# Kernel optimization log

Measured on AMD Instinct MI355X. Metric: run time of the kernel, lower is better.

The kernel has to match this reference:

```python
import jax, jax.numpy as jnp
import numpy as np

INPUT_SCALE = 1.0
TABLE_SIZE = 32
D_EMBED = 64
N = 1_000_000


def setup_inputs() -> dict:
    key = jax.random.key(0)
    k1, k2 = jax.random.split(key)
    x = jax.random.normal(k1, (N, 3), dtype=jnp.float32)
    # learned table parameter: [E, D, H, W] (batch dim of 1 dropped)
    table = jax.random.normal(k2, (D_EMBED, TABLE_SIZE, TABLE_SIZE, TABLE_SIZE), dtype=jnp.float32) * 0.1
    return {"x": x, "table": table}


def _grid_sample_3d(table, grid):
    """F.grid_sample(table[None], grid[None,None,None]) with mode='bilinear',
    padding_mode='zeros', align_corners=False.
    table: [E, D, H, W]; grid: [n, 3] with (x->W, y->H, z->D) order.
    Returns [n, E]."""
    E, Dz, Hy, Wx = table.shape
    sizes_f = jnp.array([Wx, Hy, Dz], dtype=table.dtype)
    dims_i = jnp.array([Wx, Hy, Dz], dtype=jnp.int32)
    # align_corners=False: pix = ((coord + 1) * size - 1) / 2
    pix = ((grid + 1.0) * sizes_f - 1.0) * 0.5   # [n, 3]
    p0f = jnp.floor(pix)
    frac = pix - p0f                              # [n, 3]
    p0 = p0f.astype(jnp.int32)
    tab_flat = table.reshape(E, -1).T             # [D*H*W, E]
    out = jnp.zeros((grid.shape[0], E), dtype=table.dtype)
    for dz in (0, 1):
        for dy in (0, 1):
            for dx in (0, 1):
                off = jnp.array([dx, dy, dz], dtype=jnp.int32)
                idx = p0 + off                                        # [n, 3]
                inb = jnp.all((idx >= 0) & (idx < dims_i), axis=-1)   # zeros padding
                idxc = jnp.clip(idx, 0, dims_i - 1)
                lin = (idxc[:, 2] * Hy + idxc[:, 1]) * Wx + idxc[:, 0]
                vals = tab_flat[lin]                                  # [n, E]
                w = jnp.prod(jnp.where(off == 1, frac, 1.0 - frac), axis=-1)
                out = out + vals * (w * inb.astype(table.dtype))[:, None]
    return out


def reference(x, table):
    xc = jnp.clip(x * INPUT_SCALE, -1.0, 1.0)
    return _grid_sample_3d(table, xc)
```

## Files before the change

kernel.cpp:

```cpp
#include <hip/hip_runtime.h>


constexpr int TSZ = 32;
constexpr int S   = TSZ * TSZ * TSZ;
constexpr int EMB = 64;

typedef float floatx4 __attribute__((ext_vector_type(4)));
typedef float f32x2   __attribute__((ext_vector_type(2)));

__device__ __forceinline__ unsigned short f32_to_bf16_rne(float f) {
  unsigned int u = __float_as_uint(f);
  unsigned int lsb = (u >> 16) & 1u;
  u += 0x7FFFu + lsb;
  return (unsigned short)(u >> 16);
}

__global__ __launch_bounds__(256) void transpose_table_k(
    const float* __restrict__ tab, unsigned short* __restrict__ tabT) {
  __shared__ float tile[EMB][EMB + 1];
  const int s_base = blockIdx.x * 64;
  const int t  = threadIdx.x;
  const int c0 = t & 63;
  const int r0 = t >> 6;
#pragma unroll
  for (int i = 0; i < 16; ++i) {
    const int e = r0 + 4 * i;
    tile[e][c0] = tab[(size_t)e * S + (s_base + c0)];
  }
  __syncthreads();
  const int hv = c0 >> 5;
  const int ch = c0 & 31;
#pragma unroll
  for (int i = 0; i < 16; ++i) {
    const int s = r0 + 4 * i;
    tabT[(size_t)hv * S * 32 + (size_t)(s_base + s) * 32 + ch] =
        f32_to_bf16_rne(tile[c0][s]);
  }
}

__global__ __launch_bounds__(256) void embed_k(
    const float* __restrict__ x, const uint4* __restrict__ tabT,
    float* __restrict__ out, int n, int nchunks) {
  const int bid = blockIdx.x;
  const int hv    = (bid >> 2) & 1;
  const int chunk = (bid >> 3) * 4 + (bid & 3);
  if (chunk >= nchunks) return;
  const int t  = threadIdx.x;
  const int pt = chunk * 64 + (t >> 2);
  if (pt >= n) return;
  const int o  = t & 3;

  const float gx = fminf(fmaxf(__builtin_nontemporal_load(&x[3 * pt + 0]), -1.f), 1.f);
  const float gy = fminf(fmaxf(__builtin_nontemporal_load(&x[3 * pt + 1]), -1.f), 1.f);
  const float gz = fminf(fmaxf(__builtin_nontemporal_load(&x[3 * pt + 2]), -1.f), 1.f);
  const float px = ((gx + 1.f) * 32.f - 1.f) * 0.5f;
  const float py = ((gy + 1.f) * 32.f - 1.f) * 0.5f;
  const float pz = ((gz + 1.f) * 32.f - 1.f) * 0.5f;

  const float fxf = floorf(px), fyf = floorf(py), fzf = floorf(pz);
  const int ix0 = (int)fxf, iy0 = (int)fyf, iz0 = (int)fzf;
  const float fx = px - fxf, fy = py - fyf, fz = pz - fzf;

  float wxe[2], wye[2], wze[2];
  int   ixc[2], iyc[2], izc[2];
  wxe[0] = (ix0 >= 0)       ? (1.f - fx) : 0.f;
  wxe[1] = (ix0 + 1 < TSZ)  ? fx         : 0.f;
  ixc[0] = max(ix0, 0);
  ixc[1] = min(ix0 + 1, TSZ - 1);
  wye[0] = (iy0 >= 0)       ? (1.f - fy) : 0.f;
  wye[1] = (iy0 + 1 < TSZ)  ? fy         : 0.f;
  iyc[0] = max(iy0, 0);
  iyc[1] = min(iy0 + 1, TSZ - 1);
  wze[0] = (iz0 >= 0)       ? (1.f - fz) : 0.f;
  wze[1] = (iz0 + 1 < TSZ)  ? fz         : 0.f;
  izc[0] = max(iz0, 0);
  izc[1] = min(iz0 + 1, TSZ - 1);

  const uint4* tb = tabT + (size_t)hv * (S * 4);

  f32x2 a01 = {0.f, 0.f}, a23 = {0.f, 0.f}, a45 = {0.f, 0.f}, a67 = {0.f, 0.f};

#pragma unroll
  for (int dz = 0; dz < 2; ++dz) {
    const int zb = izc[dz] * (TSZ * TSZ);
#pragma unroll
    for (int dy = 0; dy < 2; ++dy) {
      const int   zyb = zb + iyc[dy] * TSZ;
      const float wzy = wze[dz] * wye[dy];
#pragma unroll
      for (int dx = 0; dx < 2; ++dx) {
        const float w   = wzy * wxe[dx];
        const int   lin = zyb + ixc[dx];
        const uint4 q   = tb[lin * 4 + o];
        const f32x2 w2  = {w, w};
        const f32x2 v01 = {__uint_as_float(q.x << 16),
                           __uint_as_float(q.x & 0xFFFF0000u)};
        const f32x2 v23 = {__uint_as_float(q.y << 16),
                           __uint_as_float(q.y & 0xFFFF0000u)};
        const f32x2 v45 = {__uint_as_float(q.z << 16),
                           __uint_as_float(q.z & 0xFFFF0000u)};
        const f32x2 v67 = {__uint_as_float(q.w << 16),
                           __uint_as_float(q.w & 0xFFFF0000u)};
        a01 = __builtin_elementwise_fma(v01, w2, a01);
        a23 = __builtin_elementwise_fma(v23, w2, a23);
        a45 = __builtin_elementwise_fma(v45, w2, a45);
        a67 = __builtin_elementwise_fma(v67, w2, a67);
      }
    }
  }

  const floatx4 s0 = {a01.x, a01.y, a23.x, a23.y};
  const floatx4 s1 = {a45.x, a45.y, a67.x, a67.y};
  float* dstp = out + (size_t)pt * EMB + hv * 32 + o * 8;
  __builtin_nontemporal_store(s0, (floatx4*)dstp);
  __builtin_nontemporal_store(s1, (floatx4*)(dstp + 4));
}

__global__ __launch_bounds__(256) void embed_fallback_k(
    const float* __restrict__ x, const float* __restrict__ tab,
    float* __restrict__ out, int n) {
  const int gid = blockIdx.x * 256 + threadIdx.x;
  const int pt  = gid >> 6;
  if (pt >= n) return;
  const int e = gid & 63;

  const float gx = fminf(fmaxf(x[3 * pt + 0], -1.f), 1.f);
  const float gy = fminf(fmaxf(x[3 * pt + 1], -1.f), 1.f);
  const float gz = fminf(fmaxf(x[3 * pt + 2], -1.f), 1.f);
  const float px = ((gx + 1.f) * 32.f - 1.f) * 0.5f;
  const float py = ((gy + 1.f) * 32.f - 1.f) * 0.5f;
  const float pz = ((gz + 1.f) * 32.f - 1.f) * 0.5f;

  const float fxf = floorf(px), fyf = floorf(py), fzf = floorf(pz);
  const int ix0 = (int)fxf, iy0 = (int)fyf, iz0 = (int)fzf;
  const float fx = px - fxf, fy = py - fyf, fz = pz - fzf;
  const float wx[2] = {1.f - fx, fx};
  const float wy[2] = {1.f - fy, fy};
  const float wz[2] = {1.f - fz, fz};

  float acc = 0.f;
#pragma unroll
  for (int dz = 0; dz < 2; ++dz) {
    const int  iz  = iz0 + dz;
    const bool bz  = (unsigned)iz < (unsigned)TSZ;
    const int  izc = min(max(iz, 0), TSZ - 1);
#pragma unroll
    for (int dy = 0; dy < 2; ++dy) {
      const int  iy  = iy0 + dy;
      const bool by  = (unsigned)iy < (unsigned)TSZ;
      const int  iyc = min(max(iy, 0), TSZ - 1);
#pragma unroll
      for (int dx = 0; dx < 2; ++dx) {
        const int  ix  = ix0 + dx;
        const bool bx  = (unsigned)ix < (unsigned)TSZ;
        const int  ixc = min(max(ix, 0), TSZ - 1);
        float w = wz[dz] * wy[dy] * wx[dx];
        w = (bx && by && bz) ? w : 0.f;
        const int lin = (izc * TSZ + iyc) * TSZ + ixc;
        acc = fmaf(w, tab[(size_t)e * S + lin], acc);
      }
    }
  }
  out[(size_t)pt * EMB + e] = acc;
}

extern "C" void kernel_launch(void* const* d_in, const int* in_sizes, int n_in,
                              void* d_out, int out_size, void* d_ws,
                              size_t ws_size, hipStream_t stream) {
  const float* x   = (const float*)d_in[0];
  const float* tab = (const float*)d_in[1];
  float*       out = (float*)d_out;
  const int n = in_sizes[0] / 3;

  const size_t need = (size_t)S * EMB * sizeof(unsigned short);
  if (ws_size >= need) {
    unsigned short* tabT = (unsigned short*)d_ws;
    transpose_table_k<<<S / 64, 256, 0, stream>>>(tab, tabT);
    const int C = (n + 63) / 64;
    const int G = ((2 * C + 7) / 8) * 8;
    embed_k<<<G, 256, 0, stream>>>(x, (const uint4*)tabT, out, n, C);
  } else {
    const int total  = n * EMB;
    const int blocks = (total + 255) / 256;
    embed_fallback_k<<<blocks, 256, 0, stream>>>(x, tab, out, n);
  }
}
```

Measured before the change: 336.8 us.

## Store bf16 table as full 64-wide rows and map eight threads per point

The transposed bf16 table now keeps each voxel's 64 channels in one contiguous 128-byte row instead of two 32-channel halves. The embed kernel assigns eight threads to each point, so every trilinear corner becomes a single contiguous 128-byte gather. Coordinates and weights are loaded and computed once per point instead of once per half. Accumulators are rearranged with wave shuffles so each thread writes two 16-byte pieces that form contiguous output segments across its group, at the cost of extra shuffle instructions.

```diff
diff --git a/kernel.cpp b/kernel.cpp
--- a/kernel.cpp
+++ b/kernel.cpp
@@ -28,27 +28,20 @@
     tile[e][c0] = tab[(size_t)e * S + (s_base + c0)];
   }
   __syncthreads();
-  const int hv = c0 >> 5;
-  const int ch = c0 & 31;
 #pragma unroll
   for (int i = 0; i < 16; ++i) {
     const int s = r0 + 4 * i;
-    tabT[(size_t)hv * S * 32 + (size_t)(s_base + s) * 32 + ch] =
-        f32_to_bf16_rne(tile[c0][s]);
+    tabT[(size_t)(s_base + s) * EMB + c0] = f32_to_bf16_rne(tile[c0][s]);
   }
 }
 
 __global__ __launch_bounds__(256) void embed_k(
     const float* __restrict__ x, const uint4* __restrict__ tabT,
-    float* __restrict__ out, int n, int nchunks) {
-  const int bid = blockIdx.x;
-  const int hv    = (bid >> 2) & 1;
-  const int chunk = (bid >> 3) * 4 + (bid & 3);
-  if (chunk >= nchunks) return;
-  const int t  = threadIdx.x;
-  const int pt = chunk * 64 + (t >> 2);
+    float* __restrict__ out, int n) {
+  const int gid = blockIdx.x * 256 + threadIdx.x;
+  const int pt  = gid >> 3;
   if (pt >= n) return;
-  const int o  = t & 3;
+  const int c8 = gid & 7;
 
   const float gx = fminf(fmaxf(__builtin_nontemporal_load(&x[3 * pt + 0]), -1.f), 1.f);
   const float gy = fminf(fmaxf(__builtin_nontemporal_load(&x[3 * pt + 1]), -1.f), 1.f);
@@ -76,8 +69,6 @@
   izc[0] = max(iz0, 0);
   izc[1] = min(iz0 + 1, TSZ - 1);
 
-  const uint4* tb = tabT + (size_t)hv * (S * 4);
-
   f32x2 a01 = {0.f, 0.f}, a23 = {0.f, 0.f}, a45 = {0.f, 0.f}, a67 = {0.f, 0.f};
 
 #pragma unroll
@@ -91,7 +82,7 @@
       for (int dx = 0; dx < 2; ++dx) {
         const float w   = wzy * wxe[dx];
         const int   lin = zyb + ixc[dx];
-        const uint4 q   = tb[lin * 4 + o];
+        const uint4 q   = tabT[lin * 8 + c8];
         const f32x2 w2  = {w, w};
         const f32x2 v01 = {__uint_as_float(q.x << 16),
                            __uint_as_float(q.x & 0xFFFF0000u)};
@@ -109,11 +100,27 @@
     }
   }
 
-  const floatx4 s0 = {a01.x, a01.y, a23.x, a23.y};
-  const floatx4 s1 = {a45.x, a45.y, a67.x, a67.y};
-  float* dstp = out + (size_t)pt * EMB + hv * 32 + o * 8;
-  __builtin_nontemporal_store(s0, (floatx4*)dstp);
-  __builtin_nontemporal_store(s1, (floatx4*)(dstp + 4));
+  const float accv[8] = {a01.x, a01.y, a23.x, a23.y, a45.x, a45.y, a67.x, a67.y};
+  const int lane = threadIdx.x & 63;
+  const int grp  = lane & ~7;
+  const int src1 = grp + (c8 >> 1);
+  const int src2 = grp + 4 + (c8 >> 1);
+  const bool hi  = (c8 & 1) != 0;
+  float o0[4], o1[4];
+#pragma unroll
+  for (int j = 0; j < 4; ++j) {
+    const float aj = __shfl(accv[j],     src1, 64);
+    const float bj = __shfl(accv[4 + j], src1, 64);
+    o0[j] = hi ? bj : aj;
+    const float cj = __shfl(accv[j],     src2, 64);
+    const float dj = __shfl(accv[4 + j], src2, 64);
+    o1[j] = hi ? dj : cj;
+  }
+  const floatx4 s0 = {o0[0], o0[1], o0[2], o0[3]};
+  const floatx4 s1 = {o1[0], o1[1], o1[2], o1[3]};
+  float* rowp = out + (size_t)pt * EMB;
+  __builtin_nontemporal_store(s0, (floatx4*)(rowp + c8 * 4));
+  __builtin_nontemporal_store(s1, (floatx4*)(rowp + 32 + c8 * 4));
 }
 
 __global__ __launch_bounds__(256) void embed_fallback_k(
@@ -176,9 +183,9 @@
   if (ws_size >= need) {
     unsigned short* tabT = (unsigned short*)d_ws;
     transpose_table_k<<<S / 64, 256, 0, stream>>>(tab, tabT);
-    const int C = (n + 63) / 64;
-    const int G = ((2 * C + 7) / 8) * 8;
-    embed_k<<<G, 256, 0, stream>>>(x, (const uint4*)tabT, out, n, C);
+    const int total  = n * 8;
+    const int blocks = (total + 255) / 256;
+    embed_k<<<blocks, 256, 0, stream>>>(x, (const uint4*)tabT, out, n);
   } else {
     const int total  = n * EMB;
     const int blocks = (total + 255) / 256;
```

Measured after the change: 309.2 us, median of 2. 1.09x faster.
